# Optimization experiments

Measured on AMD Instinct MI355X. Metric: run time of the kernel, lower is better.

Reference implementation:

```python
import jax, jax.numpy as jnp
import numpy as np

EPS_PIXEL = 1e-8
EPS_INST = 1e-5  # torch InstanceNorm2d default
NEG_SLOPE = 0.2


def setup_inputs() -> dict:
    key = jax.random.key(0)
    k1, k2, k3, k4, k5, k6 = jax.random.split(key, 6)
    B, C, H, W, S = 16, 512, 64, 64, 512
    x = jax.random.normal(k1, (B, C, H, W), dtype=jnp.float32)
    noise = jax.random.normal(k2, (B, 1, H, W), dtype=jnp.float32)
    style = jax.random.normal(k3, (B, S), dtype=jnp.float32)
    # NoiseLayer weight initialized to zeros in torch; use small random to exercise grads
    noise_weight = jax.random.normal(k4, (C,), dtype=jnp.float32) * 0.1
    lin_W = jax.random.normal(k5, (S, 2 * C), dtype=jnp.float32) / jnp.sqrt(S).astype(jnp.float32)
    lin_b = jax.random.normal(k6, (2 * C,), dtype=jnp.float32) * 0.01
    return {"x": x, "noise": noise, "style": style,
            "noise_weight": noise_weight, "lin_W": lin_W, "lin_b": lin_b}


def reference(x, noise, style, noise_weight, lin_W, lin_b):
    # Noise: per-pixel noise, per-channel weight
    x = x + noise_weight[None, :, None, None] * noise  # [B,C,H,W]
    # Activation: LeakyReLU(0.2)
    x = jnp.where(x >= 0, x, NEG_SLOPE * x)
    # PixelNorm: normalize by RMS over channel dim
    x = x * jax.lax.rsqrt(jnp.mean(x * x, axis=1, keepdims=True) + EPS_PIXEL)
    # InstanceNorm2d (affine=False): normalize over spatial dims per (b, c)
    mean = jnp.mean(x, axis=(2, 3), keepdims=True)
    var = jnp.mean(jnp.square(x - mean), axis=(2, 3), keepdims=True)
    x = (x - mean) * jax.lax.rsqrt(var + EPS_INST)
    # StyleMod: linear -> [B, 2, C], scale-shift
    s = style @ lin_W + lin_b            # [B, 2C]
    s = s.reshape(x.shape[0], 2, x.shape[1], 1, 1)
    return x * (s[:, 0] + 1.0) + s[:, 1]
```

## Files before the change

kernel.cpp:

```cpp
#include <hip/hip_runtime.h>


#define BB 16
#define CC 512
#define HWN 4096
#define HW4 1024
#define KSPLIT 64
#define CPB (CC / KSPLIT)
#define NSTYLE 256

#define EPS_PIXEL 1e-8f
#define EPS_INST 1e-5f

__global__ __launch_bounds__(256) void k1_partials(
        const float* __restrict__ x,
        const float* __restrict__ noise,
        const float* __restrict__ nw,
        const float* __restrict__ style,
        const float* __restrict__ lin_W,
        const float* __restrict__ lin_b,
        float* __restrict__ partial,
        float* __restrict__ sp) {
    const int bid = blockIdx.x;
    const int t = threadIdx.x;

    if (bid < NSTYLE) {
        const int b  = bid >> 4;
        const int jg = (bid >> 2) & 3;
        const int z  = bid & 3;
        const int j  = jg * 256 + t;
        __shared__ float ssty[128];
        if (t < 128) ssty[t] = style[b * 512 + z * 128 + t];
        __syncthreads();
        float acc = (z == 0) ? lin_b[j] : 0.0f;
        const float* Wp = lin_W + (size_t)(z * 128) * 1024 + j;
#pragma unroll 8
        for (int k = 0; k < 128; ++k)
            acc = fmaf(ssty[k], Wp[(size_t)k * 1024], acc);
        sp[(size_t)(b * 4 + z) * 1024 + j] = acc;
        return;
    }

    const int pb = bid - NSTYLE;
    const int b  = pb >> 6;
    const int cs = pb & 63;
    const int c0 = cs * CPB;

    const float4* x4 = (const float4*)x;
    const float4* n4 = (const float4*)noise + (size_t)b * HW4;

    float4 nz[4], acc[4];
#pragma unroll
    for (int i = 0; i < 4; ++i) {
        nz[i] = n4[t + 256 * i];
        acc[i] = make_float4(0.f, 0.f, 0.f, 0.f);
    }

#pragma unroll
    for (int cci = 0; cci < CPB; ++cci) {
        const int c = c0 + cci;
        const float w = nw[c];
        const float4* xp = x4 + (size_t)(b * CC + c) * HW4;
#pragma unroll
        for (int i = 0; i < 4; ++i) {
            float4 v = xp[t + 256 * i];
            float y0 = fmaf(w, nz[i].x, v.x); y0 = fmaxf(y0, 0.2f * y0);
            float y1 = fmaf(w, nz[i].y, v.y); y1 = fmaxf(y1, 0.2f * y1);
            float y2 = fmaf(w, nz[i].z, v.z); y2 = fmaxf(y2, 0.2f * y2);
            float y3 = fmaf(w, nz[i].w, v.w); y3 = fmaxf(y3, 0.2f * y3);
            acc[i].x = fmaf(y0, y0, acc[i].x);
            acc[i].y = fmaf(y1, y1, acc[i].y);
            acc[i].z = fmaf(y2, y2, acc[i].z);
            acc[i].w = fmaf(y3, y3, acc[i].w);
        }
    }

    float4* pp = (float4*)partial + (size_t)(b * KSPLIT + cs) * HW4;
#pragma unroll
    for (int i = 0; i < 4; ++i)
        pp[t + 256 * i] = acc[i];
}

__global__ __launch_bounds__(256) void pixel_reduce(
        const float* __restrict__ partial,
        float* __restrict__ rbuf) {
    const int bid = blockIdx.x;
    const int b  = bid >> 4;
    const int qb = (bid & 15) * 64;
    const int t = threadIdx.x;
    const int ql = t & 63;
    const int kq = t >> 6;

    const float4* p4 = (const float4*)partial;
    float4 s = make_float4(0.f, 0.f, 0.f, 0.f);
    const int q = qb + ql;
#pragma unroll
    for (int kk = 0; kk < 16; ++kk) {
        const int k = kq * 16 + kk;
        float4 v = p4[(size_t)(b * KSPLIT + k) * HW4 + q];
        s.x += v.x; s.y += v.y; s.z += v.z; s.w += v.w;
    }
    __shared__ float4 red[256];
    red[t] = s;
    __syncthreads();
    if (t < 64) {
        float4 a0 = red[t], a1 = red[t + 64], a2 = red[t + 128], a3 = red[t + 192];
        float sx = a0.x + a1.x + a2.x + a3.x;
        float sy = a0.y + a1.y + a2.y + a3.y;
        float sz = a0.z + a1.z + a2.z + a3.z;
        float sw = a0.w + a1.w + a2.w + a3.w;
        const float inv_c = 1.0f / (float)CC;
        float4 o;
        o.x = rsqrtf(fmaf(sx, inv_c, EPS_PIXEL));
        o.y = rsqrtf(fmaf(sy, inv_c, EPS_PIXEL));
        o.z = rsqrtf(fmaf(sz, inv_c, EPS_PIXEL));
        o.w = rsqrtf(fmaf(sw, inv_c, EPS_PIXEL));
        ((float4*)rbuf)[b * HW4 + qb + t] = o;
    }
}

__global__ __launch_bounds__(256) void fused_apply(
        const float* __restrict__ x,
        const float* __restrict__ noise,
        const float* __restrict__ nw,
        const float* __restrict__ rbuf,
        const float* __restrict__ sp,
        float* __restrict__ out) {
    const int bid = blockIdx.x;
    const int b = bid >> 9;
    const int c = bid & 511;
    const int t = threadIdx.x;
    const float w = nw[c];

    float s0p = 0.f, s1p = 0.f;
    if (t == 0) {
#pragma unroll
        for (int z = 0; z < 4; ++z) {
            s0p += sp[(size_t)(b * 4 + z) * 1024 + c];
            s1p += sp[(size_t)(b * 4 + z) * 1024 + 512 + c];
        }
    }

    const float4* x4 = (const float4*)x + (size_t)(b * CC + c) * HW4;
    const float4* n4 = (const float4*)noise + (size_t)b * HW4;
    const float4* r4 = (const float4*)rbuf + (size_t)b * HW4;

    float4 zv[4];
    float sum = 0.f, sum2 = 0.f;
#pragma unroll
    for (int i = 0; i < 4; ++i) {
        const int q = t + 256 * i;
        float4 v = x4[q];
        float4 nz = n4[q];
        float4 rr = r4[q];
        float y0 = fmaf(w, nz.x, v.x); y0 = fmaxf(y0, 0.2f * y0);
        float y1 = fmaf(w, nz.y, v.y); y1 = fmaxf(y1, 0.2f * y1);
        float y2 = fmaf(w, nz.z, v.z); y2 = fmaxf(y2, 0.2f * y2);
        float y3 = fmaf(w, nz.w, v.w); y3 = fmaxf(y3, 0.2f * y3);
        float4 zz;
        zz.x = y0 * rr.x; zz.y = y1 * rr.y; zz.z = y2 * rr.z; zz.w = y3 * rr.w;
        zv[i] = zz;
        sum  += zz.x + zz.y + zz.z + zz.w;
        sum2 = fmaf(zz.x, zz.x, sum2);
        sum2 = fmaf(zz.y, zz.y, sum2);
        sum2 = fmaf(zz.z, zz.z, sum2);
        sum2 = fmaf(zz.w, zz.w, sum2);
    }

    __shared__ float lds[16];
#pragma unroll
    for (int off = 32; off > 0; off >>= 1) {
        sum  += __shfl_down(sum, off, 64);
        sum2 += __shfl_down(sum2, off, 64);
    }
    const int lane = t & 63, wv = t >> 6;
    if (lane == 0) { lds[wv] = sum; lds[8 + wv] = sum2; }
    __syncthreads();
    if (t == 0) {
        float S1 = lds[0] + lds[1] + lds[2] + lds[3];
        float S2 = lds[8] + lds[9] + lds[10] + lds[11];
        float m = S1 * (1.0f / (float)HWN);
        float var = fmaf(-m, m, S2 * (1.0f / (float)HWN));
        float istd = rsqrtf(var + EPS_INST);
        float A = istd * (s0p + 1.0f);
        lds[12] = A;
        lds[13] = fmaf(-m, A, s1p);
    }
    __syncthreads();
    const float A = lds[12];
    const float Bs = lds[13];

    float4* o4 = (float4*)out + (size_t)(b * CC + c) * HW4;
#pragma unroll
    for (int i = 0; i < 4; ++i) {
        const int q = t + 256 * i;
        float4 zz = zv[i];
        float4 o;
        o.x = fmaf(zz.x, A, Bs);
        o.y = fmaf(zz.y, A, Bs);
        o.z = fmaf(zz.z, A, Bs);
        o.w = fmaf(zz.w, A, Bs);
        o4[q] = o;
    }
}

extern "C" void kernel_launch(void* const* d_in, const int* in_sizes, int n_in,
                              void* d_out, int out_size, void* d_ws, size_t ws_size,
                              hipStream_t stream) {
    const float* x      = (const float*)d_in[0];
    const float* noise  = (const float*)d_in[1];
    const float* style  = (const float*)d_in[2];
    const float* nw     = (const float*)d_in[3];
    const float* lin_W  = (const float*)d_in[4];
    const float* lin_b  = (const float*)d_in[5];
    float* out = (float*)d_out;
    float* ws  = (float*)d_ws;

    float* sp   = ws;
    float* rbuf = ws + 65536;
    float* partial = out;

    k1_partials<<<NSTYLE + BB * KSPLIT, 256, 0, stream>>>(
        x, noise, nw, style, lin_W, lin_b, partial, sp);
    pixel_reduce<<<256, 256, 0, stream>>>(partial, rbuf);
    fused_apply<<<BB * CC, 256, 0, stream>>>(x, noise, nw, rbuf, sp, out);
}
```

Measured before the change: 266.1 us.

## Fuse pixel-norm partial sums and reduction into one stats kernel

The first kernel now reduces each 64-pixel column over all 512 channels inside one block, with four wavefronts of 128 channels each combined in shared memory. This removes the partial-sum buffer write and read and the separate pixel_reduce launch. The x reads become scalar 256-byte row segments strided by HWN, which may lower memory efficiency compared with the previous float4 loads. The output stores in fused_apply also switch to nontemporal stores.

```diff
diff --git a/kernel.cpp b/kernel.cpp
--- a/kernel.cpp
+++ b/kernel.cpp
@@ -5,21 +5,22 @@
 #define CC 512
 #define HWN 4096
 #define HW4 1024
-#define KSPLIT 64
-#define CPB (CC / KSPLIT)
 #define NSTYLE 256
+#define NPIX (BB * 64)
 
 #define EPS_PIXEL 1e-8f
 #define EPS_INST 1e-5f
 
-__global__ __launch_bounds__(256) void k1_partials(
+typedef float vf4 __attribute__((ext_vector_type(4)));
+
+__global__ __launch_bounds__(256) void k1_stats(
         const float* __restrict__ x,
         const float* __restrict__ noise,
         const float* __restrict__ nw,
         const float* __restrict__ style,
         const float* __restrict__ lin_W,
         const float* __restrict__ lin_b,
-        float* __restrict__ partial,
+        float* __restrict__ rbuf,
         float* __restrict__ sp) {
     const int bid = blockIdx.x;
     const int t = threadIdx.x;
@@ -41,81 +42,36 @@
         return;
     }
 
-    const int pb = bid - NSTYLE;
-    const int b  = pb >> 6;
-    const int cs = pb & 63;
-    const int c0 = cs * CPB;
+    const int pb  = bid - NSTYLE;
+    const int b   = pb >> 6;
+    const int hw0 = (pb & 63) * 64;
+    const int p   = t & 63;
+    const int g   = t >> 6;
 
-    const float4* x4 = (const float4*)x;
-    const float4* n4 = (const float4*)noise + (size_t)b * HW4;
+    __shared__ float snw[CC];
+    snw[t] = nw[t];
+    snw[t + 256] = nw[t + 256];
+    __syncthreads();
 
-    float4 nz[4], acc[4];
-#pragma unroll
-    for (int i = 0; i < 4; ++i) {
-        nz[i] = n4[t + 256 * i];
-        acc[i] = make_float4(0.f, 0.f, 0.f, 0.f);
+    const float nz = noise[b * HWN + hw0 + p];
+    const float* xp = x + ((size_t)(b * CC + g * 128) * HWN) + hw0 + p;
+
+    float acc = 0.0f;
+#pragma unroll 8
+    for (int k = 0; k < 128; ++k) {
+        float v = xp[(size_t)k * HWN];
+        float w = snw[g * 128 + k];
+        float y = fmaf(w, nz, v);
+        y = fmaxf(y, 0.2f * y);
+        acc = fmaf(y, y, acc);
     }
 
-#pragma unroll
-    for (int cci = 0; cci < CPB; ++cci) {
-        const int c = c0 + cci;
-        const float w = nw[c];
-        const float4* xp = x4 + (size_t)(b * CC + c) * HW4;
-#pragma unroll
-        for (int i = 0; i < 4; ++i) {
-            float4 v = xp[t + 256 * i];
-            float y0 = fmaf(w, nz[i].x, v.x); y0 = fmaxf(y0, 0.2f * y0);
-            float y1 = fmaf(w, nz[i].y, v.y); y1 = fmaxf(y1, 0.2f * y1);
-            float y2 = fmaf(w, nz[i].z, v.z); y2 = fmaxf(y2, 0.2f * y2);
-            float y3 = fmaf(w, nz[i].w, v.w); y3 = fmaxf(y3, 0.2f * y3);
-            acc[i].x = fmaf(y0, y0, acc[i].x);
-            acc[i].y = fmaf(y1, y1, acc[i].y);
-            acc[i].z = fmaf(y2, y2, acc[i].z);
-            acc[i].w = fmaf(y3, y3, acc[i].w);
-        }
-    }
-
-    float4* pp = (float4*)partial + (size_t)(b * KSPLIT + cs) * HW4;
-#pragma unroll
-    for (int i = 0; i < 4; ++i)
-        pp[t + 256 * i] = acc[i];
-}
-
-__global__ __launch_bounds__(256) void pixel_reduce(
-        const float* __restrict__ partial,
-        float* __restrict__ rbuf) {
-    const int bid = blockIdx.x;
-    const int b  = bid >> 4;
-    const int qb = (bid & 15) * 64;
-    const int t = threadIdx.x;
-    const int ql = t & 63;
-    const int kq = t >> 6;
-
-    const float4* p4 = (const float4*)partial;
-    float4 s = make_float4(0.f, 0.f, 0.f, 0.f);
-    const int q = qb + ql;
-#pragma unroll
-    for (int kk = 0; kk < 16; ++kk) {
-        const int k = kq * 16 + kk;
-        float4 v = p4[(size_t)(b * KSPLIT + k) * HW4 + q];
-        s.x += v.x; s.y += v.y; s.z += v.z; s.w += v.w;
-    }
-    __shared__ float4 red[256];
-    red[t] = s;
+    __shared__ float red[256];
+    red[t] = acc;
     __syncthreads();
     if (t < 64) {
-        float4 a0 = red[t], a1 = red[t + 64], a2 = red[t + 128], a3 = red[t + 192];
-        float sx = a0.x + a1.x + a2.x + a3.x;
-        float sy = a0.y + a1.y + a2.y + a3.y;
-        float sz = a0.z + a1.z + a2.z + a3.z;
-        float sw = a0.w + a1.w + a2.w + a3.w;
-        const float inv_c = 1.0f / (float)CC;
-        float4 o;
-        o.x = rsqrtf(fmaf(sx, inv_c, EPS_PIXEL));
-        o.y = rsqrtf(fmaf(sy, inv_c, EPS_PIXEL));
-        o.z = rsqrtf(fmaf(sz, inv_c, EPS_PIXEL));
-        o.w = rsqrtf(fmaf(sw, inv_c, EPS_PIXEL));
-        ((float4*)rbuf)[b * HW4 + qb + t] = o;
+        float s = red[t] + red[t + 64] + red[t + 128] + red[t + 192];
+        rbuf[b * HWN + hw0 + t] = rsqrtf(fmaf(s, 1.0f / (float)CC, EPS_PIXEL));
     }
 }
 
@@ -190,17 +146,17 @@
     const float A = lds[12];
     const float Bs = lds[13];
 
-    float4* o4 = (float4*)out + (size_t)(b * CC + c) * HW4;
+    vf4* o4 = (vf4*)out + (size_t)(b * CC + c) * HW4;
 #pragma unroll
     for (int i = 0; i < 4; ++i) {
         const int q = t + 256 * i;
         float4 zz = zv[i];
-        float4 o;
+        vf4 o;
         o.x = fmaf(zz.x, A, Bs);
         o.y = fmaf(zz.y, A, Bs);
         o.z = fmaf(zz.z, A, Bs);
         o.w = fmaf(zz.w, A, Bs);
-        o4[q] = o;
+        __builtin_nontemporal_store(o, o4 + q);
     }
 }
 
@@ -218,10 +174,8 @@
 
     float* sp   = ws;
     float* rbuf = ws + 65536;
-    float* partial = out;
 
-    k1_partials<<<NSTYLE + BB * KSPLIT, 256, 0, stream>>>(
-        x, noise, nw, style, lin_W, lin_b, partial, sp);
-    pixel_reduce<<<256, 256, 0, stream>>>(partial, rbuf);
+    k1_stats<<<NSTYLE + NPIX, 256, 0, stream>>>(
+        x, noise, nw, style, lin_W, lin_b, rbuf, sp);
     fused_apply<<<BB * CC, 256, 0, stream>>>(x, noise, nw, rbuf, sp, out);
 }
```

After: 257.9 us. 3.1% less time.
